# Kernel optimization log

Hardware: AMD Instinct MI355X
Metric: run time of the kernel (lower is better)

## Reference

```python
import jax, jax.numpy as jnp
import numpy as np

T, B, IN, H1, H2, OUT = 1024, 512, 20, 128, 64, 3

def _uniform(key, shape, bound):
    return jax.random.uniform(key, shape, jnp.float32, -bound, bound)

def setup_inputs() -> dict:
    key = jax.random.key(0)
    ks = jax.random.split(key, 11)
    b1 = 1.0 / np.sqrt(H1)
    b2 = 1.0 / np.sqrt(H2)
    return {
        "x": jax.random.normal(ks[0], (T, B, IN), jnp.float32),
        "W_ih0": _uniform(ks[1], (4 * H1, IN), b1),
        "W_hh0": _uniform(ks[2], (4 * H1, H1), b1),
        "b_ih0": _uniform(ks[3], (4 * H1,), b1),
        "b_hh0": _uniform(ks[4], (4 * H1,), b1),
        "W_ih1": _uniform(ks[5], (4 * H2, H1), b2),
        "W_hh1": _uniform(ks[6], (4 * H2, H2), b2),
        "b_ih1": _uniform(ks[7], (4 * H2,), b2),
        "b_hh1": _uniform(ks[8], (4 * H2,), b2),
        "W_d": _uniform(ks[9], (OUT, H2), b2),
        "b_d": _uniform(ks[10], (OUT,), b2),
    }

def _lstm_layer(x, W_ih, W_hh, b_ih, b_hh, hidden):
    # x: (T, B, in_dim); PyTorch gate order: i, f, g, o
    batch = x.shape[1]
    x_proj = jnp.einsum("tbi,gi->tbg", x, W_ih) + (b_ih + b_hh)  # (T,B,4H)

    def step(carry, xp):
        h, c = carry
        gates = xp + h @ W_hh.T  # (B,4H)
        i, f, g, o = jnp.split(gates, 4, axis=-1)
        i = jax.nn.sigmoid(i)
        f = jax.nn.sigmoid(f)
        g = jnp.tanh(g)
        o = jax.nn.sigmoid(o)
        c = f * c + i * g
        h = o * jnp.tanh(c)
        return (h, c), h

    h0 = jnp.zeros((batch, hidden), x.dtype)
    c0 = jnp.zeros((batch, hidden), x.dtype)
    _, ys = jax.lax.scan(step, (h0, c0), x_proj)
    return ys  # (T, B, H)

def reference(x, W_ih0, W_hh0, b_ih0, b_hh0, W_ih1, W_hh1, b_ih1, b_hh1, W_d, b_d):
    h1 = _lstm_layer(x, W_ih0, W_hh0, b_ih0, b_hh0, H1)   # (T,B,128)
    h2 = _lstm_layer(h1, W_ih1, W_hh1, b_ih1, b_hh1, H2)  # (T,B,64)
    # Faithful to original: lstm_out[:, -1, :] in seq-first layout picks the
    # last batch element at every timestep -> (T, 64)
    last = h2[:, -1, :]
    act = jax.nn.relu(last)
    # Dropout in eval mode is identity.
    return act @ W_d.T + b_d  # (T, 3)
```

## Files before the change

### kernel.cpp

```cpp
#include <hip/hip_runtime.h>
#include <hip/hip_bf16.h>


#define T_STEPS 1024
#define BATCH   512
#define IN_F    20
#define H1_     128
#define H2_     64
#define OUT_F   3
#define G1_     (4*H1_)
#define G2_     (4*H2_)

typedef float f4 __attribute__((ext_vector_type(4)));
typedef float f2 __attribute__((ext_vector_type(2)));
typedef unsigned int u32;
typedef u32 u4 __attribute__((ext_vector_type(4)));
typedef _Float16 h2t __attribute__((ext_vector_type(2)));

__device__ __forceinline__ float sigmoidf_(float x) {
    return 1.0f / (1.0f + __expf(-x));
}
__device__ __forceinline__ float tanhf_(float x) {
    return 1.0f - 2.0f / (__expf(2.0f * x) + 1.0f);
}
__device__ __forceinline__ h2t as_h2(u32 v) {
    union { u32 u; h2t h; } c; c.u = v; return c.h;
}
__device__ __forceinline__ u32 pkh(float a, float b) {
    union { _Float16 h[2]; u32 u; } c;
    c.h[0] = (_Float16)a; c.h[1] = (_Float16)b; return c.u;
}
__device__ __forceinline__ float fdot2_(h2t a, h2t b, float c) {
#if __has_builtin(__builtin_amdgcn_fdot2)
    return __builtin_amdgcn_fdot2(a, b, c, false);
#else
    float d = c;
    asm("v_dot2_f32_f16 %0, %1, %2, %0" : "+v"(d) : "v"(a), "v"(b));
    return d;
#endif
}
__device__ __forceinline__ u4 packq(const float* p) {
    const f4 a = *(const f4*)p;
    const f4 b = *(const f4*)(p + 4);
    u4 pk;
    pk.x = pkh(a.x, a.y); pk.y = pkh(a.z, a.w);
    pk.z = pkh(b.x, b.y); pk.w = pkh(b.z, b.w);
    return pk;
}

#define LO_SCALE_INV 0.000244140625f

#define DOTQ4(WQ, HH, HL, A0, A1, A2, A3)                                     \
    { A0 = fdot2_(as_h2((WQ).x), as_h2((HH).x), A0);                          \
      A1 = fdot2_(as_h2((WQ).y), as_h2((HH).y), A1);                          \
      A0 = fdot2_(as_h2((WQ).z), as_h2((HH).z), A0);                          \
      A1 = fdot2_(as_h2((WQ).w), as_h2((HH).w), A1);                          \
      A2 = fdot2_(as_h2((WQ).x), as_h2((HL).x), A2);                          \
      A3 = fdot2_(as_h2((WQ).y), as_h2((HL).y), A3);                          \
      A2 = fdot2_(as_h2((WQ).z), as_h2((HL).z), A2);                          \
      A3 = fdot2_(as_h2((WQ).w), as_h2((HL).w), A3); }

__global__ void xproj_kernel(const float* __restrict__ x,
                             const float* __restrict__ W_ih0,
                             const float* __restrict__ b_ih0,
                             const float* __restrict__ b_hh0,
                             float* __restrict__ xp1)
{
    const int t = blockIdx.x;
    const int g = threadIdx.x;
    const float* xr = x + ((size_t)t * BATCH + (BATCH - 1)) * IN_F;
    const float* w  = W_ih0 + g * IN_F;
    float acc = b_ih0[g] + b_hh0[g];
#pragma unroll
    for (int i = 0; i < IN_F; ++i) acc = fmaf(xr[i], w[i], acc);
    xp1[t * G1_ + g] = acc;
}

__global__ void pack_kernel(const float* __restrict__ W_hh0,
                            const float* __restrict__ W_hh1,
                            u4* __restrict__ wpk1,
                            u4* __restrict__ wpk2)
{
    const int idx = blockIdx.x * blockDim.x + threadIdx.x;
    if (idx < 8192) {
        const int q = idx >> 10, v = idx & 1023;
        const int r = v & 255, qf = v >> 8;
        const int g = 2 * r + (q >> 2);
        wpk1[idx] = packq(W_hh0 + (size_t)g * H1_ + qf * 32 + (q & 3) * 8);
    } else if (idx < 8192 + 2048) {
        const int i2 = idx - 8192;
        const int q = i2 >> 10, v2 = i2 & 1023;
        const int g2 = v2 & 255, qf2 = v2 >> 8;
        wpk2[i2] = packq(W_hh1 + (size_t)g2 * H2_ + qf2 * 16 + q * 8);
    }
}

__global__ __attribute__((amdgpu_flat_work_group_size(1024, 1024),
                          amdgpu_waves_per_eu(4, 4)))
void lstm1_kernel(const float* __restrict__ xp1,
                  const u4* __restrict__ wpk1,
                  float* __restrict__ h1seq)
{
    const int tid = threadIdx.x;
    const int r   = tid & 255;
    const int qf  = tid >> 8;

    __shared__ u4    shhi[16];
    __shared__ u4    shlo[16];
    __shared__ float sp1[G1_ * 5];

    if (tid < 16) { shhi[tid] = u4{0,0,0,0}; shlo[tid] = u4{0,0,0,0}; }
    float c1 = 0.0f;
    __syncthreads();

    const u4* wb = wpk1 + tid;
    f2 xp_cur = f2{0.f, 0.f};
    if (qf == 0) xp_cur = *(const f2*)(xp1 + 2 * r);

    for (int t = 0; t < T_STEPS; ++t) {
        f2 xp_next = f2{0.f, 0.f};
        if (qf == 0) {
            const int tn = (t + 1 < T_STEPS) ? (t + 1) : (T_STEPS - 1);
            xp_next = *(const f2*)(xp1 + (size_t)tn * G1_ + 2 * r);
        }
        const u4 wa0 = wb[0 * 1024], wa1 = wb[1 * 1024];
        const u4 wa2 = wb[2 * 1024], wa3 = wb[3 * 1024];
        const u4 wb0 = wb[4 * 1024], wb1 = wb[5 * 1024];
        const u4 wb2 = wb[6 * 1024], wb3 = wb[7 * 1024];
        const u4 hh0 = shhi[qf * 4 + 0], hl0 = shlo[qf * 4 + 0];
        const u4 hh1 = shhi[qf * 4 + 1], hl1 = shlo[qf * 4 + 1];
        const u4 hh2 = shhi[qf * 4 + 2], hl2 = shlo[qf * 4 + 2];
        const u4 hh3 = shhi[qf * 4 + 3], hl3 = shlo[qf * 4 + 3];

        float a0 = 0.f, a1 = 0.f, a2 = 0.f, a3 = 0.f;
        float b0 = 0.f, b1 = 0.f, b2 = 0.f, b3 = 0.f;
        DOTQ4(wa0, hh0, hl0, a0, a1, a2, a3);
        DOTQ4(wa1, hh1, hl1, a0, a1, a2, a3);
        DOTQ4(wa2, hh2, hl2, a0, a1, a2, a3);
        DOTQ4(wa3, hh3, hl3, a0, a1, a2, a3);
        DOTQ4(wb0, hh0, hl0, b0, b1, b2, b3);
        DOTQ4(wb1, hh1, hl1, b0, b1, b2, b3);
        DOTQ4(wb2, hh2, hl2, b0, b1, b2, b3);
        DOTQ4(wb3, hh3, hl3, b0, b1, b2, b3);

        sp1[(2 * r)     * 5 + qf] = ((a0 + a1) + LO_SCALE_INV * (a2 + a3)) + xp_cur.x;
        sp1[(2 * r + 1) * 5 + qf] = ((b0 + b1) + LO_SCALE_INV * (b2 + b3)) + xp_cur.y;
        __syncthreads();

        if (tid < H1_) {
            const int j = tid;
            const float* s0 = sp1 + j * 5;
            const float* s1 = sp1 + (H1_ + j) * 5;
            const float* s2 = sp1 + (2 * H1_ + j) * 5;
            const float* s3 = sp1 + (3 * H1_ + j) * 5;
            const float vi = (s0[0] + s0[1]) + (s0[2] + s0[3]);
            const float vf = (s1[0] + s1[1]) + (s1[2] + s1[3]);
            const float vg = (s2[0] + s2[1]) + (s2[2] + s2[3]);
            const float vo = (s3[0] + s3[1]) + (s3[2] + s3[3]);
            c1 = fmaf(sigmoidf_(vf), c1, sigmoidf_(vi) * tanhf_(vg));
            const float h = sigmoidf_(vo) * tanhf_(c1);
            const _Float16 hh16 = (_Float16)h;
            const float hrem = (h - (float)hh16) * 4096.0f;
            ((_Float16*)shhi)[j] = hh16;
            ((_Float16*)shlo)[j] = (_Float16)hrem;
            h1seq[(size_t)t * H1_ + j] = h;
        }
        __syncthreads();
        xp_cur = xp_next;
    }
}

__global__ void xproj2_kernel(const float* __restrict__ h1seq,
                              const float* __restrict__ W_ih1,
                              const float* __restrict__ b_ih1,
                              const float* __restrict__ b_hh1,
                              float* __restrict__ xp2)
{
    const int t = blockIdx.x;
    const int g = threadIdx.x;
    __shared__ f4 sh[H1_ / 4];
    if (g < H1_ / 4) sh[g] = ((const f4*)(h1seq + (size_t)t * H1_))[g];
    __syncthreads();
    const f4* w = (const f4*)(W_ih1 + (size_t)g * H1_);
    float ax = 0.f, ay = 0.f, az = 0.f, aw = 0.f;
#pragma unroll
    for (int k = 0; k < H1_ / 4; ++k) {
        const f4 h4 = sh[k]; const f4 w4 = w[k];
        ax = fmaf(w4.x, h4.x, ax); ay = fmaf(w4.y, h4.y, ay);
        az = fmaf(w4.z, h4.z, az); aw = fmaf(w4.w, h4.w, aw);
    }
    xp2[(size_t)t * G2_ + g] = ((ax + ay) + (az + aw)) + b_ih1[g] + b_hh1[g];
}

__global__ __attribute__((amdgpu_flat_work_group_size(1024, 1024),
                          amdgpu_waves_per_eu(4, 4)))
void lstm2_kernel(const float* __restrict__ xp2,
                  const u4* __restrict__ wpk2,
                  float* __restrict__ h2seq)
{
    const int tid = threadIdx.x;
    const int g2  = tid & 255;
    const int qf  = tid >> 8;

    __shared__ u4    shhi[8];
    __shared__ u4    shlo[8];
    __shared__ float sp2[1024];

    if (tid < 8) { shhi[tid] = u4{0,0,0,0}; shlo[tid] = u4{0,0,0,0}; }
    float c2 = 0.0f;
    __syncthreads();

    const u4* wb = wpk2 + tid;
    float xp_cur = (qf == 0) ? xp2[g2] : 0.0f;

    for (int t = 0; t < T_STEPS; ++t) {
        float xp_next = 0.0f;
        if (qf == 0) {
            const int tn = (t + 1 < T_STEPS) ? (t + 1) : (T_STEPS - 1);
            xp_next = xp2[(size_t)tn * G2_ + g2];
        }
        const u4 w0_ = wb[0], w1_ = wb[1024];
        const u4 hh0 = shhi[qf * 2 + 0], hl0 = shlo[qf * 2 + 0];
        const u4 hh1 = shhi[qf * 2 + 1], hl1 = shlo[qf * 2 + 1];

        float a0 = 0.f, a1 = 0.f, a2 = 0.f, a3 = 0.f;
        DOTQ4(w0_, hh0, hl0, a0, a1, a2, a3);
        DOTQ4(w1_, hh1, hl1, a0, a1, a2, a3);

        sp2[g2 * 4 + qf] = ((a0 + a1) + LO_SCALE_INV * (a2 + a3)) + xp_cur;
        __syncthreads();

        if (tid < H2_) {
            const f4 pi = ((const f4*)sp2)[tid];
            const f4 pf = ((const f4*)sp2)[H2_ + tid];
            const f4 pg = ((const f4*)sp2)[2 * H2_ + tid];
            const f4 po = ((const f4*)sp2)[3 * H2_ + tid];
            const float vi = (pi.x + pi.y) + (pi.z + pi.w);
            const float vf = (pf.x + pf.y) + (pf.z + pf.w);
            const float vg = (pg.x + pg.y) + (pg.z + pg.w);
            const float vo = (po.x + po.y) + (po.z + po.w);
            c2 = fmaf(sigmoidf_(vf), c2, sigmoidf_(vi) * tanhf_(vg));
            const float h = sigmoidf_(vo) * tanhf_(c2);
            const _Float16 hh16 = (_Float16)h;
            const float hrem = (h - (float)hh16) * 4096.0f;
            ((_Float16*)shhi)[tid] = hh16;
            ((_Float16*)shlo)[tid] = (_Float16)hrem;
            h2seq[(size_t)t * H2_ + tid] = h;
        }
        __syncthreads();
        xp_cur = xp_next;
    }
}

__global__ void head_kernel(const float* __restrict__ h2seq,
                            const float* __restrict__ W_d,
                            const float* __restrict__ b_d,
                            float* __restrict__ out)
{
    const int idx = blockIdx.x * blockDim.x + threadIdx.x;
    if (idx >= T_STEPS * OUT_F) return;
    const int t = idx / OUT_F;
    const int o = idx - t * OUT_F;
    const float* hr = h2seq + (size_t)t * H2_;
    const float* w  = W_d + o * H2_;
    float acc = b_d[o];
#pragma unroll
    for (int j = 0; j < H2_; ++j) acc = fmaf(fmaxf(hr[j], 0.0f), w[j], acc);
    out[idx] = acc;
}

extern "C" void kernel_launch(void* const* d_in, const int* in_sizes, int n_in,
                              void* d_out, int out_size, void* d_ws, size_t ws_size,
                              hipStream_t stream) {
    const float* x     = (const float*)d_in[0];
    const float* W_ih0 = (const float*)d_in[1];
    const float* W_hh0 = (const float*)d_in[2];
    const float* b_ih0 = (const float*)d_in[3];
    const float* b_hh0 = (const float*)d_in[4];
    const float* W_ih1 = (const float*)d_in[5];
    const float* W_hh1 = (const float*)d_in[6];
    const float* b_ih1 = (const float*)d_in[7];
    const float* b_hh1 = (const float*)d_in[8];
    const float* W_d   = (const float*)d_in[9];
    const float* b_d   = (const float*)d_in[10];

    float* out   = (float*)d_out;
    float* xp1   = (float*)d_ws;
    float* h1seq = xp1 + (size_t)T_STEPS * G1_;
    float* h2seq = h1seq + (size_t)T_STEPS * H1_;
    u4*    wpk1  = (u4*)(h2seq + (size_t)T_STEPS * H2_);
    u4*    wpk2  = wpk1 + 8192;
    float* xp2   = xp1;

    hipLaunchKernelGGL(xproj_kernel, dim3(T_STEPS), dim3(G1_), 0, stream,
                       x, W_ih0, b_ih0, b_hh0, xp1);
    hipLaunchKernelGGL(pack_kernel, dim3(40), dim3(256), 0, stream,
                       W_hh0, W_hh1, wpk1, wpk2);
    hipLaunchKernelGGL(lstm1_kernel, dim3(1), dim3(1024), 0, stream,
                       xp1, wpk1, h1seq);
    hipLaunchKernelGGL(xproj2_kernel, dim3(T_STEPS), dim3(G2_), 0, stream,
                       h1seq, W_ih1, b_ih1, b_hh1, xp2);
    hipLaunchKernelGGL(lstm2_kernel, dim3(1), dim3(1024), 0, stream,
                       xp2, wpk2, h2seq);
    hipLaunchKernelGGL(head_kernel, dim3((T_STEPS * OUT_F + 255) / 256), dim3(256),
                       0, stream, h2seq, W_d, b_d, out);
}
```

Baseline: 1.657 ms.

## Keep recurrent weights register-resident and shrink LSTM blocks to 256 threads

Both recurrent LSTM kernels now run 256 threads per block instead of 1024. Each thread holds its full packed W_hh row slice in registers, loaded once before the time loop, rather than refetching weights from global memory every step. Because a single thread now covers the whole K dimension, the four-way partial-sum reduction through shared memory goes away and the gate buffer shrinks. In exchange each thread does 4x more dot products per step with fewer waves to hide latency, and the register pressure (32 u4 per thread in lstm1) risks spilling.

```diff
diff --git a/kernel.cpp b/kernel.cpp
--- a/kernel.cpp
+++ b/kernel.cpp
@@ -49,6 +49,9 @@
 }
 
 #define LO_SCALE_INV 0.000244140625f
+
+#define REPQ8(M)  M(0) M(1) M(2) M(3) M(4) M(5) M(6) M(7)
+#define REPQ16(M) REPQ8(M) M(8) M(9) M(10) M(11) M(12) M(13) M(14) M(15)
 
 #define DOTQ4(WQ, HH, HL, A0, A1, A2, A3)                                     \
     { A0 = fdot2_(as_h2((WQ).x), as_h2((HH).x), A0);                          \
@@ -83,90 +86,89 @@
 {
     const int idx = blockIdx.x * blockDim.x + threadIdx.x;
     if (idx < 8192) {
-        const int q = idx >> 10, v = idx & 1023;
-        const int r = v & 255, qf = v >> 8;
-        const int g = 2 * r + (q >> 2);
-        wpk1[idx] = packq(W_hh0 + (size_t)g * H1_ + qf * 32 + (q & 3) * 8);
+        const int q = idx >> 8, r = idx & 255;
+        const int g = 2 * r + (q >> 4);
+        wpk1[idx] = packq(W_hh0 + (size_t)g * H1_ + (q & 15) * 8);
     } else if (idx < 8192 + 2048) {
         const int i2 = idx - 8192;
-        const int q = i2 >> 10, v2 = i2 & 1023;
-        const int g2 = v2 & 255, qf2 = v2 >> 8;
-        wpk2[i2] = packq(W_hh1 + (size_t)g2 * H2_ + qf2 * 16 + q * 8);
+        const int q = i2 >> 8, r = i2 & 255;
+        wpk2[i2] = packq(W_hh1 + (size_t)r * H2_ + q * 8);
     }
 }
 
-__global__ __attribute__((amdgpu_flat_work_group_size(1024, 1024),
-                          amdgpu_waves_per_eu(4, 4)))
+__global__ __attribute__((amdgpu_flat_work_group_size(256, 256),
+                          amdgpu_waves_per_eu(1, 1)))
 void lstm1_kernel(const float* __restrict__ xp1,
                   const u4* __restrict__ wpk1,
                   float* __restrict__ h1seq)
 {
     const int tid = threadIdx.x;
-    const int r   = tid & 255;
-    const int qf  = tid >> 8;
 
     __shared__ u4    shhi[16];
     __shared__ u4    shlo[16];
-    __shared__ float sp1[G1_ * 5];
+    __shared__ float sg[G1_];
+
+#define LWA(k) u4 wA##k = wpk1[(k) * 256 + tid];
+    REPQ16(LWA)
+#undef LWA
+#define LWB(k) u4 wB##k = wpk1[((k) + 16) * 256 + tid];
+    REPQ16(LWB)
+#undef LWB
+    asm volatile("" : "+v"(wA0), "+v"(wA1), "+v"(wA2), "+v"(wA3),
+                      "+v"(wA4), "+v"(wA5), "+v"(wA6), "+v"(wA7),
+                      "+v"(wA8), "+v"(wA9), "+v"(wA10), "+v"(wA11),
+                      "+v"(wA12), "+v"(wA13), "+v"(wA14), "+v"(wA15));
+    asm volatile("" : "+v"(wB0), "+v"(wB1), "+v"(wB2), "+v"(wB3),
+                      "+v"(wB4), "+v"(wB5), "+v"(wB6), "+v"(wB7),
+                      "+v"(wB8), "+v"(wB9), "+v"(wB10), "+v"(wB11),
+                      "+v"(wB12), "+v"(wB13), "+v"(wB14), "+v"(wB15));
 
     if (tid < 16) { shhi[tid] = u4{0,0,0,0}; shlo[tid] = u4{0,0,0,0}; }
     float c1 = 0.0f;
     __syncthreads();
 
-    const u4* wb = wpk1 + tid;
-    f2 xp_cur = f2{0.f, 0.f};
-    if (qf == 0) xp_cur = *(const f2*)(xp1 + 2 * r);
+    f2 xpv = *(const f2*)(xp1 + 2 * tid);
 
     for (int t = 0; t < T_STEPS; ++t) {
-        f2 xp_next = f2{0.f, 0.f};
-        if (qf == 0) {
+        f2 xpn;
+        {
             const int tn = (t + 1 < T_STEPS) ? (t + 1) : (T_STEPS - 1);
-            xp_next = *(const f2*)(xp1 + (size_t)tn * G1_ + 2 * r);
+            xpn = *(const f2*)(xp1 + (size_t)tn * G1_ + 2 * tid);
         }
-        const u4 wa0 = wb[0 * 1024], wa1 = wb[1 * 1024];
-        const u4 wa2 = wb[2 * 1024], wa3 = wb[3 * 1024];
-        const u4 wb0 = wb[4 * 1024], wb1 = wb[5 * 1024];
-        const u4 wb2 = wb[6 * 1024], wb3 = wb[7 * 1024];
-        const u4 hh0 = shhi[qf * 4 + 0], hl0 = shlo[qf * 4 + 0];
-        const u4 hh1 = shhi[qf * 4 + 1], hl1 = shlo[qf * 4 + 1];
-        const u4 hh2 = shhi[qf * 4 + 2], hl2 = shlo[qf * 4 + 2];
-        const u4 hh3 = shhi[qf * 4 + 3], hl3 = shlo[qf * 4 + 3];
+#define LH(k) const u4 hh##k = shhi[k]; const u4 hl##k = shlo[k];
+        REPQ16(LH)
+#undef LH
 
         float a0 = 0.f, a1 = 0.f, a2 = 0.f, a3 = 0.f;
         float b0 = 0.f, b1 = 0.f, b2 = 0.f, b3 = 0.f;
-        DOTQ4(wa0, hh0, hl0, a0, a1, a2, a3);
-        DOTQ4(wa1, hh1, hl1, a0, a1, a2, a3);
-        DOTQ4(wa2, hh2, hl2, a0, a1, a2, a3);
-        DOTQ4(wa3, hh3, hl3, a0, a1, a2, a3);
-        DOTQ4(wb0, hh0, hl0, b0, b1, b2, b3);
-        DOTQ4(wb1, hh1, hl1, b0, b1, b2, b3);
-        DOTQ4(wb2, hh2, hl2, b0, b1, b2, b3);
-        DOTQ4(wb3, hh3, hl3, b0, b1, b2, b3);
-
-        sp1[(2 * r)     * 5 + qf] = ((a0 + a1) + LO_SCALE_INV * (a2 + a3)) + xp_cur.x;
-        sp1[(2 * r + 1) * 5 + qf] = ((b0 + b1) + LO_SCALE_INV * (b2 + b3)) + xp_cur.y;
+#define DA(k) DOTQ4(wA##k, hh##k, hl##k, a0, a1, a2, a3)
+        REPQ16(DA)
+#undef DA
+#define DB(k) DOTQ4(wB##k, hh##k, hl##k, b0, b1, b2, b3)
+        REPQ16(DB)
+#undef DB
+
+        f2 gv;
+        gv.x = ((a0 + a1) + LO_SCALE_INV * (a2 + a3)) + xpv.x;
+        gv.y = ((b0 + b1) + LO_SCALE_INV * (b2 + b3)) + xpv.y;
+        *(f2*)(sg + 2 * tid) = gv;
         __syncthreads();
 
         if (tid < H1_) {
-            const int j = tid;
-            const float* s0 = sp1 + j * 5;
-            const float* s1 = sp1 + (H1_ + j) * 5;
-            const float* s2 = sp1 + (2 * H1_ + j) * 5;
-            const float* s3 = sp1 + (3 * H1_ + j) * 5;
-            const float vi = (s0[0] + s0[1]) + (s0[2] + s0[3]);
-            const float vf = (s1[0] + s1[1]) + (s1[2] + s1[3]);
-            const float vg = (s2[0] + s2[1]) + (s2[2] + s2[3]);
-            const float vo = (s3[0] + s3[1]) + (s3[2] + s3[3]);
+            const float vi = sg[tid];
+            const float vf = sg[H1_ + tid];
+            const float vg = sg[2 * H1_ + tid];
+            const float vo = sg[3 * H1_ + tid];
             c1 = fmaf(sigmoidf_(vf), c1, sigmoidf_(vi) * tanhf_(vg));
             const float h = sigmoidf_(vo) * tanhf_(c1);
             const _Float16 hh16 = (_Float16)h;
             const float hrem = (h - (float)hh16) * 4096.0f;
-            ((_Float16*)shhi)[j] = hh16;
-            ((_Float16*)shlo)[j] = (_Float16)hrem;
-            h1seq[(size_t)t * H1_ + j] = h;
+            ((_Float16*)shhi)[tid] = hh16;
+            ((_Float16*)shlo)[tid] = (_Float16)hrem;
+            h1seq[(size_t)t * H1_ + tid] = h;
         }
         __syncthreads();
-        xp_cur = xp_next;
+        xpv = xpn;
     }
 }
 
@@ -192,53 +194,53 @@
     xp2[(size_t)t * G2_ + g] = ((ax + ay) + (az + aw)) + b_ih1[g] + b_hh1[g];
 }
 
-__global__ __attribute__((amdgpu_flat_work_group_size(1024, 1024),
-                          amdgpu_waves_per_eu(4, 4)))
+__global__ __attribute__((amdgpu_flat_work_group_size(256, 256),
+                          amdgpu_waves_per_eu(1, 1)))
 void lstm2_kernel(const float* __restrict__ xp2,
                   const u4* __restrict__ wpk2,
                   float* __restrict__ h2seq)
 {
     const int tid = threadIdx.x;
-    const int g2  = tid & 255;
-    const int qf  = tid >> 8;
 
     __shared__ u4    shhi[8];
     __shared__ u4    shlo[8];
-    __shared__ float sp2[1024];
+    __shared__ float sg2[G2_];
+
+#define LW2(k) u4 w##k = wpk2[(k) * 256 + tid];
+    REPQ8(LW2)
+#undef LW2
+    asm volatile("" : "+v"(w0), "+v"(w1), "+v"(w2), "+v"(w3),
+                      "+v"(w4), "+v"(w5), "+v"(w6), "+v"(w7));
 
     if (tid < 8) { shhi[tid] = u4{0,0,0,0}; shlo[tid] = u4{0,0,0,0}; }
     float c2 = 0.0f;
     __syncthreads();
 
-    const u4* wb = wpk2 + tid;
-    float xp_cur = (qf == 0) ? xp2[g2] : 0.0f;
+    float xp_cur = xp2[tid];
 
     for (int t = 0; t < T_STEPS; ++t) {
-        float xp_next = 0.0f;
-        if (qf == 0) {
+        float xp_next;
+        {
             const int tn = (t + 1 < T_STEPS) ? (t + 1) : (T_STEPS - 1);
-            xp_next = xp2[(size_t)tn * G2_ + g2];
+            xp_next = xp2[(size_t)tn * G2_ + tid];
         }
-        const u4 w0_ = wb[0], w1_ = wb[1024];
-        const u4 hh0 = shhi[qf * 2 + 0], hl0 = shlo[qf * 2 + 0];
-        const u4 hh1 = shhi[qf * 2 + 1], hl1 = shlo[qf * 2 + 1];
+#define LH2(k) const u4 hh##k = shhi[k]; const u4 hl##k = shlo[k];
+        REPQ8(LH2)
+#undef LH2
 
         float a0 = 0.f, a1 = 0.f, a2 = 0.f, a3 = 0.f;
-        DOTQ4(w0_, hh0, hl0, a0, a1, a2, a3);
-        DOTQ4(w1_, hh1, hl1, a0, a1, a2, a3);
-
-        sp2[g2 * 4 + qf] = ((a0 + a1) + LO_SCALE_INV * (a2 + a3)) + xp_cur;
+#define D2(k) DOTQ4(w##k, hh##k, hl##k, a0, a1, a2, a3)
+        REPQ8(D2)
+#undef D2
+
+        sg2[tid] = ((a0 + a1) + LO_SCALE_INV * (a2 + a3)) + xp_cur;
         __syncthreads();
 
         if (tid < H2_) {
-            const f4 pi = ((const f4*)sp2)[tid];
-            const f4 pf = ((const f4*)sp2)[H2_ + tid];
-            const f4 pg = ((const f4*)sp2)[2 * H2_ + tid];
-            const f4 po = ((const f4*)sp2)[3 * H2_ + tid];
-            const float vi = (pi.x + pi.y) + (pi.z + pi.w);
-            const float vf = (pf.x + pf.y) + (pf.z + pf.w);
-            const float vg = (pg.x + pg.y) + (pg.z + pg.w);
-            const float vo = (po.x + po.y) + (po.z + po.w);
+            const float vi = sg2[tid];
+            const float vf = sg2[H2_ + tid];
+            const float vg = sg2[2 * H2_ + tid];
+            const float vo = sg2[3 * H2_ + tid];
             c2 = fmaf(sigmoidf_(vf), c2, sigmoidf_(vi) * tanhf_(vg));
             const float h = sigmoidf_(vo) * tanhf_(c2);
             const _Float16 hh16 = (_Float16)h;
@@ -296,11 +298,11 @@
                        x, W_ih0, b_ih0, b_hh0, xp1);
     hipLaunchKernelGGL(pack_kernel, dim3(40), dim3(256), 0, stream,
                        W_hh0, W_hh1, wpk1, wpk2);
-    hipLaunchKernelGGL(lstm1_kernel, dim3(1), dim3(1024), 0, stream,
+    hipLaunchKernelGGL(lstm1_kernel, dim3(1), dim3(256), 0, stream,
                        xp1, wpk1, h1seq);
     hipLaunchKernelGGL(xproj2_kernel, dim3(T_STEPS), dim3(G2_), 0, stream,
                        h1seq, W_ih1, b_ih1, b_hh1, xp2);
-    hipLaunchKernelGGL(lstm2_kernel, dim3(1), dim3(1024), 0, stream,
+    hipLaunchKernelGGL(lstm2_kernel, dim3(1), dim3(256), 0, stream,
                        xp2, wpk2, h2seq);
     hipLaunchKernelGGL(head_kernel, dim3((T_STEPS * OUT_F + 255) / 256), dim3(256),
                        0, stream, h2seq, W_d, b_d, out);
```

New measurement: 1.824 ms. +10.1%, slower.
